# Kernel optimization log

Measured on AMD Instinct MI355X. Metric: run time of the kernel, lower is better.

Reference implementation:

```python
import jax, jax.numpy as jnp
import numpy as np

B, N, D = 2048, 65536, 128  # batch queries, max_engrams, spike_dim


def setup_inputs() -> dict:
    key = jax.random.key(0)
    k1, k2, k3, k4 = jax.random.split(key, 4)
    sensor_spikes = jax.random.normal(k1, (B, D), dtype=jnp.float32)
    # crystallize_skill stores sign(pattern), so keys/values are +-1 vectors
    sensor_keys = jnp.sign(jax.random.normal(k2, (N, D), dtype=jnp.float32))
    action_values = jnp.sign(jax.random.normal(k3, (N, D), dtype=jnp.float32))
    is_active = jax.random.bernoulli(k4, 0.5, (N,))
    return {
        "sensor_spikes": sensor_spikes,
        "sensor_keys": sensor_keys,
        "action_values": action_values,
        "is_active": is_active,
    }


def reference(sensor_spikes, sensor_keys, action_values, is_active):
    # similarity = x @ keys.T  -> [B, N]
    sim = jnp.einsum("bd,nd->bn", sensor_spikes.astype(jnp.float32), sensor_keys)
    # masked_fill_(~is_active, -inf)
    sim = jnp.where(is_active[None, :], sim, -jnp.inf)
    best_match_idx = jnp.argmax(sim, axis=-1)          # [B]
    confidence = jnp.max(sim, axis=-1)                 # [B] == sim[b, best_idx[b]]
    retrieved = action_values[best_match_idx]          # [B, D]
    return retrieved, confidence, best_match_idx
```

## Files before the change

kernel.cpp:

```cpp
#include <hip/hip_runtime.h>
#include <stdint.h>

typedef __attribute__((ext_vector_type(8))) short short8;
typedef __attribute__((ext_vector_type(4))) float f32x4;

#define NEG_INF (-__builtin_inff())

#define B_ROWS 2048
#define N_KEYS 65536
#define DIM    128


__device__ __forceinline__ unsigned short f2bf(float f) {
  unsigned u = __float_as_uint(f);
  u = (u + 0x7FFFu + ((u >> 16) & 1u)) >> 16;
  return (unsigned short)u;
}

__global__ __launch_bounds__(256) void convert_kernel(
    const float* __restrict__ x, const float* __restrict__ keys,
    short8* __restrict__ xi, short8* __restrict__ ki) {
  int t = blockIdx.x * 256 + threadIdx.x;
  const float* src;
  short8* dst;
  if (t < N_KEYS * 16) {
    int n = t >> 4, c = t & 15;
    src = keys + (size_t)n * DIM + c * 8;
    int tile = n >> 7, rl = n & 127;
    dst = ki + (size_t)tile * 2048 + ((rl >> 4) * 256 + c * 16 + (rl & 15));
  } else {
    t -= N_KEYS * 16;
    if (t >= B_ROWS * 16) return;
    int n = t >> 4, c = t & 15;
    src = x + (size_t)n * DIM + c * 8;
    int tile = n >> 7, rl = n & 127;
    dst = xi + (size_t)tile * 2048 + ((rl >> 4) * 256 + c * 16 + (rl & 15));
  }
  f32x4 v0 = *(const f32x4*)(src);
  f32x4 v1 = *(const f32x4*)(src + 4);
  short8 o;
  o[0] = (short)f2bf(v0[0]); o[1] = (short)f2bf(v0[1]);
  o[2] = (short)f2bf(v0[2]); o[3] = (short)f2bf(v0[3]);
  o[4] = (short)f2bf(v1[0]); o[5] = (short)f2bf(v1[1]);
  o[6] = (short)f2bf(v1[2]); o[7] = (short)f2bf(v1[3]);
  *dst = o;
}

#define GLDS(gp, lp)                                                      \
  __builtin_amdgcn_global_load_lds(                                       \
      (const __attribute__((address_space(1))) void*)(gp),                \
      (__attribute__((address_space(3))) void*)(lp), 16, 0, 0)

__global__ __launch_bounds__(256, 2) void sim_kernel(
    const short8* __restrict__ xi, const short8* __restrict__ ki,
    const int* __restrict__ act, float* __restrict__ cmax) {
  __shared__ short8 As[2048];
  __shared__ short8 Bs[2048];
  __shared__ float actm[128];
  const int tid = threadIdx.x;
  const int w = tid >> 6, l = tid & 63;
  const int ntile = blockIdx.x, btile = blockIdx.y;

  const short8* ag = xi + (size_t)btile * 2048 + w * 512 + l;
  const short8* bg = ki + (size_t)ntile * 2048 + w * 512 + l;
#pragma unroll
  for (int i = 0; i < 8; i++) {
    GLDS(ag + i * 64, As + w * 512 + i * 64);
    GLDS(bg + i * 64, Bs + w * 512 + i * 64);
  }
  if (tid < 128) {
    int a = act[ntile * 128 + tid];
    actm[tid] = a ? 0.0f : NEG_INF;
  }
  __syncthreads();

  const int wr = w >> 1, wc = w & 1;
  f32x4 acc[4][4];
#pragma unroll
  for (int mi = 0; mi < 4; mi++)
#pragma unroll
    for (int ni = 0; ni < 4; ni++) acc[mi][ni] = f32x4{0.f, 0.f, 0.f, 0.f};

#pragma unroll
  for (int kk = 0; kk < 4; kk++) {
    short8 af[4], bf[4];
#pragma unroll
    for (int mi = 0; mi < 4; mi++) af[mi] = As[(wr * 4 + mi) * 256 + kk * 64 + l];
#pragma unroll
    for (int ni = 0; ni < 4; ni++) bf[ni] = Bs[(wc * 4 + ni) * 256 + kk * 64 + l];
#pragma unroll
    for (int mi = 0; mi < 4; mi++)
#pragma unroll
      for (int ni = 0; ni < 4; ni++)
        acc[mi][ni] = __builtin_amdgcn_mfma_f32_16x16x32_bf16(
            af[mi], bf[ni], acc[mi][ni], 0, 0, 0);
  }

  const int lg = l >> 4, lr = l & 15;
#pragma unroll
  for (int mi = 0; mi < 4; mi++) {
    float rm[4];
#pragma unroll
    for (int r = 0; r < 4; r++) rm[r] = NEG_INF;
#pragma unroll
    for (int ni = 0; ni < 4; ni++) {
      float m = actm[wc * 64 + ni * 16 + lr];
#pragma unroll
      for (int r = 0; r < 4; r++) rm[r] = fmaxf(rm[r], acc[mi][ni][r] + m);
    }
#pragma unroll
    for (int r = 0; r < 4; r++) {
      float v = rm[r];
      v = fmaxf(v, __shfl_xor(v, 1));
      v = fmaxf(v, __shfl_xor(v, 2));
      v = fmaxf(v, __shfl_xor(v, 4));
      v = fmaxf(v, __shfl_xor(v, 8));
      rm[r] = v;
    }
    if (lr == 0) {
      int rowbase = btile * 128 + wr * 64 + mi * 16 + lg * 4;
      int chunk = ntile * 2 + wc;
#pragma unroll
      for (int r = 0; r < 4; r++)
        cmax[(size_t)(rowbase + r) * 1024 + chunk] = rm[r];
    }
  }
}

__global__ __launch_bounds__(256) void finalize_kernel(
    const float* __restrict__ x, const float* __restrict__ keys,
    const float* __restrict__ vals, const int* __restrict__ act,
    const float* __restrict__ cmax, float* __restrict__ out) {
  __shared__ float xr[128];
  __shared__ float wred[4];
  __shared__ int cand[64];
  __shared__ int ncand;
  __shared__ int bestn_s;
  __shared__ float skeys[64 * 129];
  const int b = blockIdx.x, tid = threadIdx.x;
  if (tid < 128) xr[tid] = x[(size_t)b * 128 + tid];
  if (tid == 0) ncand = 0;
  __syncthreads();

  const float* cm = cmax + (size_t)b * 1024;
  float c0 = cm[tid], c1 = cm[tid + 256], c2 = cm[tid + 512], c3 = cm[tid + 768];
  float lm = fmaxf(fmaxf(c0, c1), fmaxf(c2, c3));
#pragma unroll
  for (int s = 1; s < 64; s <<= 1) lm = fmaxf(lm, __shfl_xor(lm, s));
  if ((tid & 63) == 0) wred[tid >> 6] = lm;
  __syncthreads();
  float M = fmaxf(fmaxf(wred[0], wred[1]), fmaxf(wred[2], wred[3]));
  float thr = M - 0.75f;

  if (c0 > thr) { int p = atomicAdd(&ncand, 1); if (p < 64) cand[p] = tid; }
  if (c1 > thr) { int p = atomicAdd(&ncand, 1); if (p < 64) cand[p] = tid + 256; }
  if (c2 > thr) { int p = atomicAdd(&ncand, 1); if (p < 64) cand[p] = tid + 512; }
  if (c3 > thr) { int p = atomicAdd(&ncand, 1); if (p < 64) cand[p] = tid + 768; }
  __syncthreads();
  int nc = ncand; if (nc > 64) nc = 64;

  double bv = -(double)__builtin_inf();
  int bn = 0x7FFFFFFF;
  for (int ci = 0; ci < nc; ci++) {
    int cch = cand[ci];
    const float* kbase = keys + (size_t)cch * 64 * 128;
#pragma unroll
    for (int i = 0; i < 32; i++) {
      int idx = tid + i * 256;
      skeys[(idx >> 7) * 129 + (idx & 127)] = kbase[idx];
    }
    __syncthreads();
    if (tid < 64) {
      int n = cch * 64 + tid;
      if (act[n] != 0) {
        const float* kr = skeys + tid * 129;
        double s = 0.0;
#pragma unroll
        for (int d = 0; d < 128; d++) s += (double)xr[d] * (double)kr[d];
        if (s > bv || (s == bv && n < bn)) { bv = s; bn = n; }
      }
    }
    __syncthreads();
  }

  if (tid < 64) {
#pragma unroll
    for (int s = 1; s < 64; s <<= 1) {
      double ov = __shfl_xor(bv, s);
      int on = __shfl_xor(bn, s);
      if (ov > bv || (ov == bv && on < bn)) { bv = ov; bn = on; }
    }
    if (tid == 0) {
      bestn_s = bn;
      out[262144 + b] = (float)bv;
      out[264192 + b] = (float)bn;
    }
  }
  __syncthreads();
  int n = bestn_s;
  if (tid < 128) out[(size_t)b * 128 + tid] = vals[(size_t)n * 128 + tid];
}

__global__ __launch_bounds__(256) void direct_kernel(
    const float* __restrict__ x, const float* __restrict__ keys,
    const float* __restrict__ vals, const int* __restrict__ act,
    float* __restrict__ out) {
  __shared__ float xr[8][128];
  __shared__ double redv[8][4];
  __shared__ int redn[8][4];
  __shared__ int bests[8];
  const int tid = threadIdx.x;
  const int r0 = blockIdx.x * 8;
  const int w = tid >> 6, l = tid & 63;
#pragma unroll
  for (int i = 0; i < 4; i++) {
    int idx = tid + i * 256;
    xr[idx >> 7][idx & 127] = x[(size_t)(r0 + (idx >> 7)) * 128 + (idx & 127)];
  }
  __syncthreads();

  double bv[8];
  int bn[8];
#pragma unroll
  for (int r = 0; r < 8; r++) { bv[r] = -(double)__builtin_inf(); bn[r] = 0x7FFFFFFF; }

  for (int n = tid; n < N_KEYS; n += 256) {
    if (act[n] == 0) continue;
    const float* kr = keys + (size_t)n * 128;
    double s[8];
#pragma unroll
    for (int r = 0; r < 8; r++) s[r] = 0.0;
    for (int d = 0; d < 128; d += 4) {
      f32x4 kv = *(const f32x4*)(kr + d);
#pragma unroll
      for (int r = 0; r < 8; r++) {
        s[r] += (double)xr[r][d] * (double)kv[0];
        s[r] += (double)xr[r][d + 1] * (double)kv[1];
        s[r] += (double)xr[r][d + 2] * (double)kv[2];
        s[r] += (double)xr[r][d + 3] * (double)kv[3];
      }
    }
#pragma unroll
    for (int r = 0; r < 8; r++)
      if (s[r] > bv[r]) { bv[r] = s[r]; bn[r] = n; }
  }

#pragma unroll
  for (int r = 0; r < 8; r++) {
    double v = bv[r]; int n = bn[r];
#pragma unroll
    for (int s = 1; s < 64; s <<= 1) {
      double ov = __shfl_xor(v, s);
      int on = __shfl_xor(n, s);
      if (ov > v || (ov == v && on < n)) { v = ov; n = on; }
    }
    if (l == 0) { redv[r][w] = v; redn[r][w] = n; }
  }
  __syncthreads();
  if (tid < 8) {
    double v = redv[tid][0]; int n = redn[tid][0];
#pragma unroll
    for (int j = 1; j < 4; j++) {
      double ov = redv[tid][j]; int on = redn[tid][j];
      if (ov > v || (ov == v && on < n)) { v = ov; n = on; }
    }
    bests[tid] = n;
    out[262144 + r0 + tid] = (float)v;
    out[264192 + r0 + tid] = (float)n;
  }
  __syncthreads();
#pragma unroll
  for (int i = 0; i < 4; i++) {
    int idx = tid + i * 256;
    int r = idx >> 7, d = idx & 127;
    out[(size_t)(r0 + r) * 128 + d] = vals[(size_t)bests[r] * 128 + d];
  }
}

extern "C" void kernel_launch(void* const* d_in, const int* in_sizes, int n_in,
                              void* d_out, int out_size, void* d_ws, size_t ws_size,
                              hipStream_t stream) {
  const float* x    = (const float*)d_in[0];
  const float* keys = (const float*)d_in[1];
  const float* vals = (const float*)d_in[2];
  const int*   act  = (const int*)d_in[3];
  float* out = (float*)d_out;

  const size_t need = (size_t)(512 * 2048 + 16 * 2048) * sizeof(short8) +
                      (size_t)2048 * 1024 * sizeof(float);
  if (ws_size >= need) {
    short8* ki   = (short8*)d_ws;
    short8* xi   = ki + 512 * 2048;
    float*  cmax = (float*)(xi + 16 * 2048);
    convert_kernel<<<4224, 256, 0, stream>>>(x, keys, xi, ki);
    sim_kernel<<<dim3(512, 16), 256, 0, stream>>>(xi, ki, act, cmax);
    finalize_kernel<<<2048, 256, 0, stream>>>(x, keys, vals, act, cmax, out);
  } else {
    direct_kernel<<<256, 256, 0, stream>>>(x, keys, vals, act, out);
  }
}
```

Before: 190.1 us.

## Fuse key bf16 conversion into sim kernel and loop over all query tiles

Drops the separate bf16 conversion of the 65536x128 key matrix and its workspace round trip. Each sim block now converts its own 128-key tile straight into LDS once, then loops over all 16 query tiles, loading the pre-converted x tiles. The partial-max buffer is transposed so each wave writes contiguous float4s, and finalize reads it with a strided per-row pattern. The grid shrinks from 8192 blocks to 512, and there is no overlap between x tile loads and MFMA work, so latency hiding may suffer.

```diff
diff --git a/kernel.cpp b/kernel.cpp
--- a/kernel.cpp
+++ b/kernel.cpp
@@ -17,25 +17,14 @@
   return (unsigned short)u;
 }
 
-__global__ __launch_bounds__(256) void convert_kernel(
-    const float* __restrict__ x, const float* __restrict__ keys,
-    short8* __restrict__ xi, short8* __restrict__ ki) {
+
+__global__ __launch_bounds__(256) void convert_x_kernel(
+    const float* __restrict__ x, short8* __restrict__ xi) {
   int t = blockIdx.x * 256 + threadIdx.x;
-  const float* src;
-  short8* dst;
-  if (t < N_KEYS * 16) {
-    int n = t >> 4, c = t & 15;
-    src = keys + (size_t)n * DIM + c * 8;
-    int tile = n >> 7, rl = n & 127;
-    dst = ki + (size_t)tile * 2048 + ((rl >> 4) * 256 + c * 16 + (rl & 15));
-  } else {
-    t -= N_KEYS * 16;
-    if (t >= B_ROWS * 16) return;
-    int n = t >> 4, c = t & 15;
-    src = x + (size_t)n * DIM + c * 8;
-    int tile = n >> 7, rl = n & 127;
-    dst = xi + (size_t)tile * 2048 + ((rl >> 4) * 256 + c * 16 + (rl & 15));
-  }
+  int tile = t >> 11, loc = t & 2047;
+  int rl = ((loc >> 8) << 4) + (loc & 15);
+  int c = (loc >> 4) & 15;
+  const float* src = x + (size_t)(tile * 128 + rl) * DIM + c * 8;
   f32x4 v0 = *(const f32x4*)(src);
   f32x4 v1 = *(const f32x4*)(src + 4);
   short8 o;
@@ -43,7 +32,7 @@
   o[2] = (short)f2bf(v0[2]); o[3] = (short)f2bf(v0[3]);
   o[4] = (short)f2bf(v1[0]); o[5] = (short)f2bf(v1[1]);
   o[6] = (short)f2bf(v1[2]); o[7] = (short)f2bf(v1[3]);
-  *dst = o;
+  xi[t] = o;
 }
 
 #define GLDS(gp, lp)                                                      \
@@ -51,78 +40,94 @@
       (const __attribute__((address_space(1))) void*)(gp),                \
       (__attribute__((address_space(3))) void*)(lp), 16, 0, 0)
 
-__global__ __launch_bounds__(256, 2) void sim_kernel(
-    const short8* __restrict__ xi, const short8* __restrict__ ki,
-    const int* __restrict__ act, float* __restrict__ cmax) {
+__global__ __launch_bounds__(256, 2) void sim2_kernel(
+    const short8* __restrict__ xi, const float* __restrict__ keys,
+    const int* __restrict__ act, float* __restrict__ cmaxT) {
+  __shared__ short8 Bs[2048];
   __shared__ short8 As[2048];
-  __shared__ short8 Bs[2048];
   __shared__ float actm[128];
   const int tid = threadIdx.x;
   const int w = tid >> 6, l = tid & 63;
-  const int ntile = blockIdx.x, btile = blockIdx.y;
-
-  const short8* ag = xi + (size_t)btile * 2048 + w * 512 + l;
-  const short8* bg = ki + (size_t)ntile * 2048 + w * 512 + l;
-#pragma unroll
-  for (int i = 0; i < 8; i++) {
-    GLDS(ag + i * 64, As + w * 512 + i * 64);
-    GLDS(bg + i * 64, Bs + w * 512 + i * 64);
+  const int ntile = blockIdx.x;
+
+  const float* kb = keys + (size_t)ntile * (128 * DIM);
+#pragma unroll
+  for (int it = 0; it < 8; ++it) {
+    int li = it * 256 + tid;
+    int rl = ((li >> 8) << 4) + (li & 15);
+    int c = (li >> 4) & 15;
+    const float* src = kb + rl * DIM + c * 8;
+    f32x4 v0 = *(const f32x4*)(src);
+    f32x4 v1 = *(const f32x4*)(src + 4);
+    short8 o;
+    o[0] = (short)f2bf(v0[0]); o[1] = (short)f2bf(v0[1]);
+    o[2] = (short)f2bf(v0[2]); o[3] = (short)f2bf(v0[3]);
+    o[4] = (short)f2bf(v1[0]); o[5] = (short)f2bf(v1[1]);
+    o[6] = (short)f2bf(v1[2]); o[7] = (short)f2bf(v1[3]);
+    Bs[li] = o;
   }
   if (tid < 128) {
-    int a = act[ntile * 128 + tid];
-    actm[tid] = a ? 0.0f : NEG_INF;
-  }
-  __syncthreads();
+    actm[tid] = act[ntile * 128 + tid] ? 0.0f : NEG_INF;
+  }
 
   const int wr = w >> 1, wc = w & 1;
-  f32x4 acc[4][4];
-#pragma unroll
-  for (int mi = 0; mi < 4; mi++)
-#pragma unroll
-    for (int ni = 0; ni < 4; ni++) acc[mi][ni] = f32x4{0.f, 0.f, 0.f, 0.f};
-
-#pragma unroll
-  for (int kk = 0; kk < 4; kk++) {
-    short8 af[4], bf[4];
-#pragma unroll
-    for (int mi = 0; mi < 4; mi++) af[mi] = As[(wr * 4 + mi) * 256 + kk * 64 + l];
-#pragma unroll
-    for (int ni = 0; ni < 4; ni++) bf[ni] = Bs[(wc * 4 + ni) * 256 + kk * 64 + l];
+  const int lg = l >> 4, lr = l & 15;
+  const short8* ag0 = xi + w * 512 + l;
+  float* cout = cmaxT + (size_t)(ntile * 2 + wc) * B_ROWS;
+
+  for (int bt = 0; bt < 16; ++bt) {
+    __syncthreads();
+    const short8* ag = ag0 + (size_t)bt * 2048;
+#pragma unroll
+    for (int i = 0; i < 8; i++)
+      GLDS(ag + i * 64, As + w * 512 + i * 64);
+    __syncthreads();
+
+    f32x4 acc[4][4];
 #pragma unroll
     for (int mi = 0; mi < 4; mi++)
 #pragma unroll
-      for (int ni = 0; ni < 4; ni++)
-        acc[mi][ni] = __builtin_amdgcn_mfma_f32_16x16x32_bf16(
-            af[mi], bf[ni], acc[mi][ni], 0, 0, 0);
-  }
-
-  const int lg = l >> 4, lr = l & 15;
-#pragma unroll
-  for (int mi = 0; mi < 4; mi++) {
-    float rm[4];
-#pragma unroll
-    for (int r = 0; r < 4; r++) rm[r] = NEG_INF;
-#pragma unroll
-    for (int ni = 0; ni < 4; ni++) {
-      float m = actm[wc * 64 + ni * 16 + lr];
-#pragma unroll
-      for (int r = 0; r < 4; r++) rm[r] = fmaxf(rm[r], acc[mi][ni][r] + m);
-    }
-#pragma unroll
-    for (int r = 0; r < 4; r++) {
-      float v = rm[r];
-      v = fmaxf(v, __shfl_xor(v, 1));
-      v = fmaxf(v, __shfl_xor(v, 2));
-      v = fmaxf(v, __shfl_xor(v, 4));
-      v = fmaxf(v, __shfl_xor(v, 8));
-      rm[r] = v;
-    }
-    if (lr == 0) {
-      int rowbase = btile * 128 + wr * 64 + mi * 16 + lg * 4;
-      int chunk = ntile * 2 + wc;
-#pragma unroll
-      for (int r = 0; r < 4; r++)
-        cmax[(size_t)(rowbase + r) * 1024 + chunk] = rm[r];
+      for (int ni = 0; ni < 4; ni++) acc[mi][ni] = f32x4{0.f, 0.f, 0.f, 0.f};
+
+#pragma unroll
+    for (int kk = 0; kk < 4; kk++) {
+      short8 af[4], bfv[4];
+#pragma unroll
+      for (int mi = 0; mi < 4; mi++) af[mi] = As[(wr * 4 + mi) * 256 + kk * 64 + l];
+#pragma unroll
+      for (int ni = 0; ni < 4; ni++) bfv[ni] = Bs[(wc * 4 + ni) * 256 + kk * 64 + l];
+#pragma unroll
+      for (int mi = 0; mi < 4; mi++)
+#pragma unroll
+        for (int ni = 0; ni < 4; ni++)
+          acc[mi][ni] = __builtin_amdgcn_mfma_f32_16x16x32_bf16(
+              af[mi], bfv[ni], acc[mi][ni], 0, 0, 0);
+    }
+
+#pragma unroll
+    for (int mi = 0; mi < 4; mi++) {
+      float rm[4];
+#pragma unroll
+      for (int r = 0; r < 4; r++) rm[r] = NEG_INF;
+#pragma unroll
+      for (int ni = 0; ni < 4; ni++) {
+        float m = actm[wc * 64 + ni * 16 + lr];
+#pragma unroll
+        for (int r = 0; r < 4; r++) rm[r] = fmaxf(rm[r], acc[mi][ni][r] + m);
+      }
+#pragma unroll
+      for (int r = 0; r < 4; r++) {
+        float v = rm[r];
+        v = fmaxf(v, __shfl_xor(v, 1));
+        v = fmaxf(v, __shfl_xor(v, 2));
+        v = fmaxf(v, __shfl_xor(v, 4));
+        v = fmaxf(v, __shfl_xor(v, 8));
+        rm[r] = v;
+      }
+      if (lr == 0) {
+        int row = bt * 128 + wr * 64 + mi * 16 + lg * 4;
+        *(f32x4*)(cout + row) = f32x4{rm[0], rm[1], rm[2], rm[3]};
+      }
     }
   }
 }
@@ -130,7 +135,7 @@
 __global__ __launch_bounds__(256) void finalize_kernel(
     const float* __restrict__ x, const float* __restrict__ keys,
     const float* __restrict__ vals, const int* __restrict__ act,
-    const float* __restrict__ cmax, float* __restrict__ out) {
+    const float* __restrict__ cmaxT, float* __restrict__ out) {
   __shared__ float xr[128];
   __shared__ float wred[4];
   __shared__ int cand[64];
@@ -142,8 +147,11 @@
   if (tid == 0) ncand = 0;
   __syncthreads();
 
-  const float* cm = cmax + (size_t)b * 1024;
-  float c0 = cm[tid], c1 = cm[tid + 256], c2 = cm[tid + 512], c3 = cm[tid + 768];
+  const float* cm = cmaxT + b;
+  float c0 = cm[(size_t)tid * B_ROWS];
+  float c1 = cm[(size_t)(tid + 256) * B_ROWS];
+  float c2 = cm[(size_t)(tid + 512) * B_ROWS];
+  float c3 = cm[(size_t)(tid + 768) * B_ROWS];
   float lm = fmaxf(fmaxf(c0, c1), fmaxf(c2, c3));
 #pragma unroll
   for (int s = 1; s < 64; s <<= 1) lm = fmaxf(lm, __shfl_xor(lm, s));
@@ -286,15 +294,14 @@
   const int*   act  = (const int*)d_in[3];
   float* out = (float*)d_out;
 
-  const size_t need = (size_t)(512 * 2048 + 16 * 2048) * sizeof(short8) +
-                      (size_t)2048 * 1024 * sizeof(float);
+  const size_t need = (size_t)16 * 2048 * sizeof(short8) +
+                      (size_t)1024 * B_ROWS * sizeof(float);
   if (ws_size >= need) {
-    short8* ki   = (short8*)d_ws;
-    short8* xi   = ki + 512 * 2048;
-    float*  cmax = (float*)(xi + 16 * 2048);
-    convert_kernel<<<4224, 256, 0, stream>>>(x, keys, xi, ki);
-    sim_kernel<<<dim3(512, 16), 256, 0, stream>>>(xi, ki, act, cmax);
-    finalize_kernel<<<2048, 256, 0, stream>>>(x, keys, vals, act, cmax, out);
+    short8* xi    = (short8*)d_ws;
+    float*  cmaxT = (float*)(xi + 16 * 2048);
+    convert_x_kernel<<<128, 256, 0, stream>>>(x, xi);
+    sim2_kernel<<<512, 256, 0, stream>>>(xi, keys, act, cmaxT);
+    finalize_kernel<<<2048, 256, 0, stream>>>(x, keys, vals, act, cmaxT, out);
   } else {
     direct_kernel<<<256, 256, 0, stream>>>(x, keys, vals, act, out);
   }
```

New measurement: 181.6 us. 1.05x faster.
